# Optimization experiments

Measured on AMD Instinct MI355X. Metric: run time of the kernel, lower is better.

Reference implementation:

```python
import jax, jax.numpy as jnp
import numpy as np

B, N, F, H, K, C = 2048, 62, 512, 128, 2, 2
EPS_BN = 1e-5
EPS_NORM = 1e-10
N_TRIL = N * (N + 1) // 2  # 1953, tril_indices incl. diagonal
FC_SIZES = [H * N, H * N // 2, H * N // 4, H * N // 8, C]  # [7936,3968,1984,992,2]


def setup_inputs() -> dict:
    key = jax.random.key(0)
    ks = jax.random.split(key, 16)
    inp = {
        "x": jax.random.normal(ks[0], (B, N, F), jnp.float32),
        "edge_weight": jax.random.uniform(ks[1], (N_TRIL,), jnp.float32),
        "bn_gamma": jnp.ones((F,), jnp.float32),
        "bn_beta": jnp.zeros((F,), jnp.float32),
        # xavier_normal for SGConv lin
        "lin_w": jax.random.normal(ks[2], (H, F), jnp.float32) * (2.0 / (F + H)) ** 0.5,
        "lin_b": jnp.zeros((H,), jnp.float32),
    }
    for i in range(4):
        fan_in, fan_out = FC_SIZES[i], FC_SIZES[i + 1]
        inp[f"fc{i}_w"] = jax.random.normal(ks[3 + i], (fan_out, fan_in), jnp.float32) * (2.0 / (fan_in + fan_out)) ** 0.5
        inp[f"fc{i}_b"] = jnp.zeros((fan_out,), jnp.float32)
    return inp


def _normalized_adj(edge_weight):
    """Build symmetric dense adjacency from tril params, normalize_matrix
    (relu + sym deg-norm), then SGConv.norm (D^-1/2 A D^-1/2; self-loops are
    already on the diagonal so add_remaining_self_loops is a no-op)."""
    xs, ys = np.tril_indices(N)
    Wm = jnp.zeros((N, N), jnp.float32).at[xs, ys].set(edge_weight)
    Wm = Wm + Wm.T - jnp.diag(jnp.diag(Wm))
    A = jax.nn.relu(Wm)
    dinv = jax.lax.rsqrt(A.sum(1) + EPS_NORM)
    A = dinv[:, None] * A * dinv[None, :]
    # SGConv normalization: deg = scatter_add over rows -> row sums
    deg = A.sum(1)
    dis = jnp.where(deg > 0, deg ** -0.5, 0.0)
    return dis[:, None] * A * dis[None, :]


def reference(x, edge_weight, bn_gamma, bn_beta, lin_w, lin_b,
              fc0_w, fc0_b, fc1_w, fc1_b, fc2_w, fc2_b, fc3_w, fc3_b):
    A = _normalized_adj(edge_weight)  # [N, N], shared across batch
    # BatchNorm1d over feature channels, stats over (batch, node) dims (train mode)
    mean = x.mean((0, 1))
    var = x.var((0, 1))
    h = (x - mean) * jax.lax.rsqrt(var + EPS_BN) * bn_gamma + bn_beta  # [B,N,F]
    # K-hop SGConv propagation == dense matmul with shared normalized adjacency
    for _ in range(K):
        h = jnp.einsum('ij,bjf->bif', A, h)
    h = h @ lin_w.T + lin_b           # [B, N, H]
    h = h.reshape(B, N * H)           # node-major flatten, matches x.view(batch,-1)
    # dropout is identity in eval mode
    for W, b in ((fc0_w, fc0_b), (fc1_w, fc1_b), (fc2_w, fc2_b)):
        h = jax.nn.relu(h @ W.T + b)
    return h @ fc3_w.T + fc3_b        # [B, C]
```

## Files before the change

kernel.cpp:

```cpp
#include <hip/hip_runtime.h>

typedef _Float16 f16;
typedef __attribute__((ext_vector_type(4))) _Float16 f16x4;
typedef __attribute__((ext_vector_type(8))) _Float16 f16x8;
typedef __attribute__((ext_vector_type(4))) float f32x4;

#define DEVI static __device__ __forceinline__

DEVI void async_copy16(const f16* g, f16* l) {
  __builtin_amdgcn_global_load_lds(
      (const __attribute__((address_space(1))) void*)g,
      (__attribute__((address_space(3))) void*)l, 16, 0, 0);
}

#define MEMPIN asm volatile("" ::: "memory")
#define RBAR __builtin_amdgcn_s_barrier()

__global__ __launch_bounds__(1024) void k_adj(const float* __restrict__ ew, float* __restrict__ out)
{
  __shared__ float sW[62][64];
  __shared__ float sT[62][64];
  __shared__ float d[62];
  const int tid = threadIdx.x;
  for (int idx = tid; idx < 62 * 62; idx += 1024) {
    int i = idx / 62, j = idx % 62;
    float w = (j <= i) ? ew[i * (i + 1) / 2 + j] : ew[j * (j + 1) / 2 + i];
    sW[i][j] = fmaxf(w, 0.f);
  }
  __syncthreads();
  if (tid < 62) {
    float s = 0.f;
    for (int j = 0; j < 62; j++) s += sW[tid][j];
    d[tid] = rsqrtf(s + 1e-10f);
  }
  __syncthreads();
  for (int idx = tid; idx < 62 * 62; idx += 1024) {
    int i = idx / 62, j = idx % 62;
    sW[i][j] *= d[i] * d[j];
  }
  __syncthreads();
  if (tid < 62) {
    float s = 0.f;
    for (int j = 0; j < 62; j++) s += sW[tid][j];
    d[tid] = (s > 0.f) ? rsqrtf(s) : 0.f;
  }
  __syncthreads();
  for (int idx = tid; idx < 62 * 62; idx += 1024) {
    int i = idx / 62, j = idx % 62;
    sW[i][j] *= d[i] * d[j];
  }
  __syncthreads();
  for (int idx = tid; idx < 62 * 64; idx += 1024) {
    int i = idx >> 6, j = idx & 63;
    float s = 0.f;
    if (j < 62) {
      for (int k = 0; k < 62; k++) s += sW[i][k] * sW[k][j];
    }
    sT[i][j] = s;
    out[idx] = s;
  }
  __syncthreads();
  if (tid < 62) {
    float s = 0.f;
    for (int j = 0; j < 62; j++) s += sT[tid][j];
    out[62 * 64 + tid] = s;
  }
}

__global__ __launch_bounds__(1024) void k_bnstats(const float* __restrict__ X, float* __restrict__ part)
{
  const int tid = threadIdx.x;
  const int c4 = (tid & 127) << 2;
  const int rg = tid >> 7;
  float sx = 0, sy = 0, sz = 0, sw = 0, qx = 0, qy = 0, qz = 0, qw = 0;
  const long r0 = (long)blockIdx.x * 496 + rg;
  for (int i = 0; i < 62; i++) {
    const float4 v = *(const float4*)(X + (r0 + 8 * i) * 512 + c4);
    sx += v.x; sy += v.y; sz += v.z; sw += v.w;
    qx += v.x * v.x; qy += v.y * v.y; qz += v.z * v.z; qw += v.w * v.w;
  }
  __shared__ float red[1024][8];
  red[tid][0] = sx; red[tid][1] = sy; red[tid][2] = sz; red[tid][3] = sw;
  red[tid][4] = qx; red[tid][5] = qy; red[tid][6] = qz; red[tid][7] = qw;
  __syncthreads();
  if (tid < 128) {
    float acc8[8];
#pragma unroll
    for (int j = 0; j < 8; j++) acc8[j] = 0.f;
#pragma unroll
    for (int g = 0; g < 8; g++)
#pragma unroll
      for (int j = 0; j < 8; j++) acc8[j] += red[g * 128 + tid][j];
    float* p = part + (long)blockIdx.x * 1024;
#pragma unroll
    for (int j = 0; j < 4; j++) p[c4 + j] = acc8[j];
#pragma unroll
    for (int j = 0; j < 4; j++) p[512 + c4 + j] = acc8[4 + j];
  }
}

__global__ __launch_bounds__(512) void k_bnfin(const float* __restrict__ part, const float* __restrict__ g,
                                               const float* __restrict__ be, float* __restrict__ ssb)
{
  const int c = threadIdx.x;
  float s = 0.f, q = 0.f;
  for (int b = 0; b < 256; b++) {
    s += part[b * 1024 + c];
    q += part[b * 1024 + 512 + c];
  }
  const float inv = 1.f / 126976.f;
  const float mean = s * inv;
  const float var = q * inv - mean * mean;
  const float sc = g[c] * rsqrtf(var + 1e-5f);
  ssb[c] = sc;
  ssb[512 + c] = be[c] - mean * sc;
}

__global__ __launch_bounds__(256) void k_foldw1(const float* __restrict__ lw, const float* __restrict__ ssb,
                                                f16* __restrict__ w1h, float* __restrict__ b1p)
{
  const int h = blockIdx.x;
  const int tid = threadIdx.x;
  float partl = 0.f;
  for (int f = tid; f < 512; f += 256) {
    const float w = lw[h * 512 + f];
    w1h[h * 512 + f] = (f16)(w * ssb[f]);
    partl += w * ssb[512 + f];
  }
  __shared__ float red[256];
  red[tid] = partl;
  __syncthreads();
  for (int s = 128; s; s >>= 1) {
    if (tid < s) red[tid] += red[tid + s];
    __syncthreads();
  }
  if (tid == 0) b1p[h] = red[0];
}

__global__ __launch_bounds__(256) void k_cvtw(const float* __restrict__ src, f16* __restrict__ dst,
                                              int N, int K, int Npad, int Kpad)
{
  const long total4 = (long)Npad * Kpad / 4;
  const int kp4 = Kpad >> 2;
  for (long i = (long)blockIdx.x * 256 + threadIdx.x; i < total4; i += (long)gridDim.x * 256) {
    const long n = i / kp4;
    const int k = (int)(i % kp4) << 2;
    f16x4 h;
    if (n < N && k < K) {
      const float4 v = *(const float4*)(src + n * K + k);
      h[0] = (f16)v.x; h[1] = (f16)v.y; h[2] = (f16)v.z; h[3] = (f16)v.w;
    } else {
      h[0] = (f16)0.f; h[1] = (f16)0.f; h[2] = (f16)0.f; h[3] = (f16)0.f;
    }
    *(f16x4*)(dst + i * 4) = h;
  }
}

__global__ __launch_bounds__(256, 4) void k_gemm_lin(
    const float* __restrict__ X, const f16* __restrict__ Bw, f16* __restrict__ Y)
{
  __shared__ f16 sA[128 * 64];
  __shared__ f16 sB[128 * 64];
  const int tid = threadIdx.x;
  const int lane = tid & 63;
  const int wave = tid >> 6;
  const int wr = wave >> 1, wc = wave & 1;
  const long rowA0 = (long)blockIdx.x * 128;

  const int srow = tid >> 3;
  const int scolb = (tid & 7) << 4;
  const int gcolb = scolb ^ ((srow & 7) << 4);
  const f16* gB = Bw + (long)srow * 512 + (gcolb >> 1);
  f16* lB = sB + srow * 64 + (scolb >> 1);

  const int ac4 = tid & 15;
  const int ar0 = tid >> 4;
  const int aswz = (ar0 & 7) << 4;
  const float* gX = X + (rowA0 + ar0) * 512 + ac4 * 4;
  char* lAbase = (char*)sA + ar0 * 128 + ((ac4 * 8) ^ aswz);

  const int frow = lane & 15;
  const int kb = (lane >> 4) << 4;
  const int rswz = (lane & 7) << 4;

  f32x4 acc[4][4] = {};

  for (int kt = 0; kt < 512; kt += 64) {
#pragma unroll
    for (int i = 0; i < 8; i++) {
      const float4 v = *(const float4*)(gX + kt + (long)(16 * i) * 512);
      f16x4 hh;
      hh[0] = (f16)v.x; hh[1] = (f16)v.y; hh[2] = (f16)v.z; hh[3] = (f16)v.w;
      *(f16x4*)(lAbase + 16 * i * 128) = hh;
    }
#pragma unroll
    for (int i = 0; i < 4; i++)
      async_copy16(gB + kt + (long)i * (32 * 512), lB + i * 2048);
    __syncthreads();
#pragma unroll
    for (int kk = 0; kk < 2; kk++) {
      f16x8 af[4], bf[4];
#pragma unroll
      for (int m = 0; m < 4; m++) {
        const int row = wr * 64 + m * 16 + frow;
        af[m] = *(const f16x8*)((const char*)sA + row * 128 + ((kk * 64 + kb) ^ rswz));
      }
#pragma unroll
      for (int n = 0; n < 4; n++) {
        const int row = wc * 64 + n * 16 + frow;
        bf[n] = *(const f16x8*)((const char*)sB + row * 128 + ((kk * 64 + kb) ^ rswz));
      }
#pragma unroll
      for (int m = 0; m < 4; m++)
#pragma unroll
        for (int n = 0; n < 4; n++)
          acc[m][n] = __builtin_amdgcn_mfma_f32_16x16x32_f16(af[m], bf[n], acc[m][n], 0, 0, 0);
    }
    __syncthreads();
  }

  const int crow = wr * 64 + ((lane >> 4) << 2);
  const int ccol = wc * 64 + (lane & 15);
#pragma unroll
  for (int n = 0; n < 4; n++) {
    const int col = ccol + n * 16;
#pragma unroll
    for (int m = 0; m < 4; m++) {
      const long gr = rowA0 + crow + m * 16;
#pragma unroll
      for (int r = 0; r < 4; r++)
        Y[(gr + r) * 128 + col] = (f16)acc[m][n][r];
    }
  }
}

__global__ __launch_bounds__(256) void k_prop(const f16* __restrict__ Y, const float* __restrict__ A2,
                                              const float* __restrict__ b1p, const float* __restrict__ lb,
                                              f16* __restrict__ Z)
{
  __shared__ float sY[62 * 128];
  __shared__ float sA[62 * 64];
  __shared__ float sR[62];
  __shared__ float sB1[128];
  __shared__ float sLB[128];
  const int tid = threadIdx.x;
  const long base = (long)blockIdx.x * 7936;
  for (int i = tid; i < 992; i += 256) {
    const f16x8 v = *(const f16x8*)(Y + base + (long)i * 8);
#pragma unroll
    for (int j = 0; j < 8; j++) sY[i * 8 + j] = (float)v[j];
    const float4 a = *(const float4*)(A2 + i * 4);
    *(float4*)&sA[i * 4] = a;
  }
  if (tid < 62) sR[tid] = A2[3968 + tid];
  if (tid >= 64 && tid < 192) sB1[tid - 64] = b1p[tid - 64];
  if (tid >= 128 && tid < 256) sLB[tid - 128] = lb[tid - 128];
  __syncthreads();
  const int h = tid & 127;
  const int ng = tid >> 7;
  float yc[62];
#pragma unroll
  for (int j = 0; j < 62; j++) yc[j] = sY[j * 128 + h];
  const float bias_h1 = sB1[h];
  const float bias_h2 = sLB[h];
  for (int n = ng; n < 62; n += 2) {
    float s = 0.f;
#pragma unroll
    for (int j = 0; j < 62; j++) s += sA[n * 64 + j] * yc[j];
    s += sR[n] * bias_h1 + bias_h2;
    Z[base + n * 128 + h] = (f16)s;
  }
}

template <int LOOPN, int MT, int NT, int KS>
__global__ __launch_bounds__(512, 2) void k_fc8(
    const f16* __restrict__ A, const f16* __restrict__ Bw, f16* __restrict__ P,
    const int K, const int kslice, const int PLD)
{
  __shared__ f16 sA[2][256 * 64];
  __shared__ f16 sB[2][256 * 64];
  const int tid = threadIdx.x;
  const int bid = blockIdx.x;
  const int xcd = bid & 7, ii = bid >> 3;
  int nt, mt, ks;
  if constexpr (NT == 16) {
    nt = xcd * 2 + (ii & 1); mt = (ii >> 1) & (MT - 1); ks = ii >> 4;
  } else {
    nt = xcd; mt = ii & (MT - 1); ks = ii >> 3;
  }
  const long rowA0 = (long)mt * 256;
  const long rowB0 = (long)nt * 256;
  const long k0 = (long)ks * kslice;

  const int srow = tid >> 3;
  const int scolb = (tid & 7) << 4;
  const int gcolb = scolb ^ ((srow & 7) << 4);
  const f16* gA = A + (rowA0 + srow) * (long)K + k0 + (gcolb >> 1);
  const f16* gB = Bw + (rowB0 + srow) * (long)K + k0 + (gcolb >> 1);

#define SGA(d, q, kt) async_copy16(gA + (kt) + (long)(q) * 64 * K, &sA[d][0] + (q) * 4096 + tid * 8)
#define SGB(d, q, kt) async_copy16(gB + (kt) + (long)(q) * 64 * K, &sB[d][0] + (q) * 4096 + tid * 8)

  const int lane = tid & 63;
  const int wave = tid >> 6;
  const int wr = wave >> 2;
  const int wc = wave & 3;
  const int frow = lane & 15;
  const int kb = (lane >> 4) << 4;
  const int rsw = (frow & 7) << 4;

  f32x4 acc[8][4] = {};
  f16x8 af[4][2], bf[4][2];

#define RDA(d, mh) do { _Pragma("unroll") for (int m_ = 0; m_ < 4; m_++) {                      \
    const int row_ = wr * 128 + (mh) * 64 + m_ * 16 + frow;                                     \
    af[m_][0] = *(const f16x8*)((const char*)&sA[d][0] + row_ * 128 + ((0 + kb) ^ rsw));        \
    af[m_][1] = *(const f16x8*)((const char*)&sA[d][0] + row_ * 128 + ((64 + kb) ^ rsw)); } } while (0)
#define RDB(d) do { _Pragma("unroll") for (int n_ = 0; n_ < 4; n_++) {                          \
    const int row_ = wc * 64 + n_ * 16 + frow;                                                  \
    bf[n_][0] = *(const f16x8*)((const char*)&sB[d][0] + row_ * 128 + ((0 + kb) ^ rsw));        \
    bf[n_][1] = *(const f16x8*)((const char*)&sB[d][0] + row_ * 128 + ((64 + kb) ^ rsw)); } } while (0)
#define QUAD(mh, nh) do { _Pragma("unroll") for (int m_ = 0; m_ < 4; m_++)                      \
    _Pragma("unroll") for (int n_ = 0; n_ < 2; n_++) {                                          \
      acc[(mh)*4+m_][(nh)*2+n_] = __builtin_amdgcn_mfma_f32_16x16x32_f16(af[m_][0], bf[(nh)*2+n_][0], acc[(mh)*4+m_][(nh)*2+n_], 0, 0, 0); \
      acc[(mh)*4+m_][(nh)*2+n_] = __builtin_amdgcn_mfma_f32_16x16x32_f16(af[m_][1], bf[(nh)*2+n_][1], acc[(mh)*4+m_][(nh)*2+n_], 0, 0, 0); } } while (0)
#define VMW8 asm volatile("s_waitcnt vmcnt(8)" ::: "memory")
#define VMW0 asm volatile("s_waitcnt vmcnt(0)" ::: "memory")
#define PRIO1 __builtin_amdgcn_s_setprio(1)
#define PRIO0 __builtin_amdgcn_s_setprio(0)

  SGA(0, 0, 0); SGA(0, 2, 0); SGB(0, 0, 0); SGB(0, 1, 0);
  SGA(0, 1, 0); SGA(0, 3, 0); SGB(0, 2, 0); SGB(0, 3, 0);
  SGA(1, 0, 64); SGA(1, 2, 64); SGB(1, 0, 64); SGB(1, 1, 64);
  SGA(1, 1, 64); SGA(1, 3, 64); SGB(1, 2, 64); SGB(1, 3, 64);

  for (int t = 0; t < LOOPN; ++t) {
    const long kt2 = (long)(t + 1) * 128;
    VMW8; MEMPIN; RBAR; MEMPIN;
    RDA(0, 0); RDB(0);
    PRIO1; QUAD(0, 0); PRIO0;
    MEMPIN; RBAR; MEMPIN;
    SGA(0, 0, kt2); SGA(0, 2, kt2); SGB(0, 0, kt2); SGB(0, 1, kt2);
    QUAD(0, 1);
    RDA(0, 1);
    QUAD(1, 0);
    MEMPIN; RBAR; MEMPIN;
    SGA(0, 1, kt2); SGA(0, 3, kt2); SGB(0, 2, kt2); SGB(0, 3, kt2);
    QUAD(1, 1);
    VMW8; MEMPIN; RBAR; MEMPIN;
    RDA(1, 0); RDB(1);
    PRIO1; QUAD(0, 0); PRIO0;
    MEMPIN; RBAR; MEMPIN;
    SGA(1, 0, kt2 + 64); SGA(1, 2, kt2 + 64); SGB(1, 0, kt2 + 64); SGB(1, 1, kt2 + 64);
    QUAD(0, 1);
    RDA(1, 1);
    QUAD(1, 0);
    MEMPIN; RBAR; MEMPIN;
    SGA(1, 1, kt2 + 64); SGA(1, 3, kt2 + 64); SGB(1, 2, kt2 + 64); SGB(1, 3, kt2 + 64);
    QUAD(1, 1);
  }
  VMW8; MEMPIN; RBAR; MEMPIN;
  RDA(0, 0); RDB(0);
  PRIO1; QUAD(0, 0); QUAD(0, 1); PRIO0;
  RDA(0, 1);
  PRIO1; QUAD(1, 0); QUAD(1, 1); PRIO0;
  VMW0; MEMPIN; RBAR; MEMPIN;
  RDA(1, 0); RDB(1);
  PRIO1; QUAD(0, 0); QUAD(0, 1); PRIO0;
  RDA(1, 1);
  PRIO1; QUAD(1, 0); QUAD(1, 1); PRIO0;

  f16* Pp = P + (long)ks * 2048 * PLD;
#pragma unroll
  for (int mi = 0; mi < 8; mi++) {
    const long r0 = rowA0 + wr * 128 + (mi >> 2) * 64 + (mi & 3) * 16 + ((lane >> 4) << 2);
#pragma unroll
    for (int n = 0; n < 4; n++) {
      const long col = rowB0 + wc * 64 + n * 16 + (lane & 15);
#pragma unroll
      for (int r = 0; r < 4; r++)
        Pp[(r0 + r) * PLD + col] = (f16)acc[mi][n][r];
    }
  }
#undef SGA
#undef SGB
#undef RDA
#undef RDB
#undef QUAD
#undef VMW8
#undef VMW0
#undef PRIO1
#undef PRIO0
}

template <int S>
__global__ __launch_bounds__(256) void k_fixs(const f16* __restrict__ P, const float* __restrict__ b,
                                              f16* __restrict__ C, int N, int realN)
{
  const long total = 2048L * N;
  const int mask = N - 1;
  const long stride = (long)gridDim.x * 256 * 8;
  for (long i = ((long)blockIdx.x * 256 + threadIdx.x) * 8; i < total; i += stride) {
    float s[8];
#pragma unroll
    for (int j = 0; j < 8; j++) s[j] = 0.f;
#pragma unroll
    for (int ps = 0; ps < S; ps++) {
      const f16x8 p = *(const f16x8*)(P + (long)ps * total + i);
#pragma unroll
      for (int j = 0; j < 8; j++) s[j] += (float)p[j];
    }
    const int col = (int)(i & mask);
    f16x8 o;
#pragma unroll
    for (int j = 0; j < 8; j++) {
      const int c = col + j;
      const float bb = (c < realN) ? b[c] : 0.f;
      o[j] = (f16)fmaxf(s[j] + bb, 0.f);
    }
    *(f16x8*)(C + i) = o;
  }
}

template <int RELU>
__global__ __launch_bounds__(256, 2) void k_gemm_f16(
    const f16* __restrict__ A, const f16* __restrict__ B,
    const float* __restrict__ bias, f16* __restrict__ C,
    int N, int K, int realN)
{
  __shared__ f16 sA[128 * 64];
  __shared__ f16 sB[128 * 64];
  const int tid = threadIdx.x;
  const int lane = tid & 63;
  const int wave = tid >> 6;
  const int wr = wave >> 1, wc = wave & 1;
  const int bid = blockIdx.x;
  const int xcd = bid & 7, idx = bid >> 3;
  const long rowA0 = (long)(xcd * 2 + (idx & 1)) * 128;
  const long rowB0 = (long)(idx >> 1) * 128;

  const int srow = tid >> 3;
  const int scolb = (tid & 7) << 4;
  const int gcolb = scolb ^ ((srow & 7) << 4);
  const f16* gA = A + (rowA0 + srow) * (long)K + (gcolb >> 1);
  const f16* gB = B + (rowB0 + srow) * (long)K + (gcolb >> 1);
  f16* lA = sA + srow * 64 + (scolb >> 1);
  f16* lB = sB + srow * 64 + (scolb >> 1);
  const long rstep = 32L * K;

  const int frow = lane & 15;
  const int kb = (lane >> 4) << 4;
  const int rswz = (lane & 7) << 4;

  f32x4 acc[4][4] = {};

  for (int kt = 0; kt < K; kt += 64) {
#pragma unroll
    for (int i = 0; i < 4; i++) {
      async_copy16(gA + kt + i * rstep, lA + i * 2048);
      async_copy16(gB + kt + i * rstep, lB + i * 2048);
    }
    __syncthreads();
#pragma unroll
    for (int kk = 0; kk < 2; kk++) {
      f16x8 af[4], bf[4];
#pragma unroll
      for (int m = 0; m < 4; m++) {
        const int row = wr * 64 + m * 16 + frow;
        af[m] = *(const f16x8*)((const char*)sA + row * 128 + ((kk * 64 + kb) ^ rswz));
      }
#pragma unroll
      for (int n = 0; n < 4; n++) {
        const int row = wc * 64 + n * 16 + frow;
        bf[n] = *(const f16x8*)((const char*)sB + row * 128 + ((kk * 64 + kb) ^ rswz));
      }
#pragma unroll
      for (int m = 0; m < 4; m++)
#pragma unroll
        for (int n = 0; n < 4; n++)
          acc[m][n] = __builtin_amdgcn_mfma_f32_16x16x32_f16(af[m], bf[n], acc[m][n], 0, 0, 0);
    }
    __syncthreads();
  }

  const int crow = wr * 64 + ((lane >> 4) << 2);
  const int ccol = wc * 64 + (lane & 15);
#pragma unroll
  for (int n = 0; n < 4; n++) {
    const int col = (int)rowB0 + ccol + n * 16;
    const float bb = (col < realN) ? bias[col] : 0.f;
#pragma unroll
    for (int m = 0; m < 4; m++) {
      const long gr = rowA0 + crow + m * 16;
#pragma unroll
      for (int r = 0; r < 4; r++) {
        float v = acc[m][n][r] + bb;
        if (RELU) v = fmaxf(v, 0.f);
        C[(gr + r) * N + col] = (f16)v;
      }
    }
  }
}

__global__ __launch_bounds__(256) void k_fc3(const f16* __restrict__ H, const float* __restrict__ W,
                                             const float* __restrict__ b, float* __restrict__ out)
{
  const int row = blockIdx.x * 4 + (threadIdx.x >> 6);
  const int lane = threadIdx.x & 63;
  const f16* h = H + (long)row * 1024;
  float a0 = 0.f, a1 = 0.f;
  for (int k = lane; k < 992; k += 64) {
    const float v = (float)h[k];
    a0 += v * W[k];
    a1 += v * W[992 + k];
  }
  for (int off = 32; off; off >>= 1) {
    a0 += __shfl_down(a0, off);
    a1 += __shfl_down(a1, off);
  }
  if (lane == 0) {
    out[row * 2 + 0] = a0 + b[0];
    out[row * 2 + 1] = a1 + b[1];
  }
}

extern "C" void kernel_launch(void* const* d_in, const int* in_sizes, int n_in,
                              void* d_out, int out_size, void* d_ws, size_t ws_size,
                              hipStream_t stream)
{
  const float* x    = (const float*)d_in[0];
  const float* ew   = (const float*)d_in[1];
  const float* bng  = (const float*)d_in[2];
  const float* bnb  = (const float*)d_in[3];
  const float* linw = (const float*)d_in[4];
  const float* linb = (const float*)d_in[5];
  const float* w0   = (const float*)d_in[6];
  const float* b0   = (const float*)d_in[7];
  const float* w1   = (const float*)d_in[8];
  const float* b1   = (const float*)d_in[9];
  const float* w2   = (const float*)d_in[10];
  const float* b2   = (const float*)d_in[11];
  const float* w3   = (const float*)d_in[12];
  const float* b3   = (const float*)d_in[13];
  float* out = (float*)d_out;
  char* ws = (char*)d_ws;

  constexpr size_t oA2  = 0;
  constexpr size_t oSS  = 16384;
  constexpr size_t oB1P = 20480;
  constexpr size_t oW1H = 20992;
  constexpr size_t oP   = 152064;
  constexpr size_t oACC = oP;
  constexpr size_t oY   = oP + 1048576;
  constexpr size_t oZ   = 33706496;
  constexpr size_t oW0H = 66212352;
  constexpr size_t WS_NEED = 131224064;
  constexpr size_t oH0  = oZ;
  constexpr size_t oW1F = oZ + 16777216;
  constexpr size_t oH1  = 67260928;
  constexpr size_t oW2F = 75649536;
  constexpr size_t oH2  = 79843840;
  if (ws_size < WS_NEED) return;

  float* A2  = (float*)(ws + oA2);
  float* acc = (float*)(ws + oACC);
  float* ssb = (float*)(ws + oSS);
  float* b1p = (float*)(ws + oB1P);
  f16* w1h = (f16*)(ws + oW1H);
  f16* Y   = (f16*)(ws + oY);
  f16* P   = (f16*)(ws + oP);
  f16* Z   = (f16*)(ws + oZ);
  f16* w0h = (f16*)(ws + oW0H);
  f16* h0  = (f16*)(ws + oH0);
  f16* w1f = (f16*)(ws + oW1F);
  f16* h1  = (f16*)(ws + oH1);
  f16* w2f = (f16*)(ws + oW2F);
  f16* h2  = (f16*)(ws + oH2);

  k_adj<<<1, 1024, 0, stream>>>(ew, A2);
  k_bnstats<<<256, 1024, 0, stream>>>(x, acc);
  k_bnfin<<<1, 512, 0, stream>>>(acc, bng, bnb, ssb);
  k_foldw1<<<128, 256, 0, stream>>>(linw, ssb, w1h, b1p);
  k_cvtw<<<1024, 256, 0, stream>>>(w0, w0h, 3968, 7936, 4096, 7936);
  k_gemm_lin<<<992, 256, 0, stream>>>(x, w1h, Y);
  k_prop<<<2048, 256, 0, stream>>>(Y, A2, b1p, linb, Z);
  k_fc8<30, 8, 16, 2><<<256, 512, 0, stream>>>(Z, w0h, P, 7936, 3968, 4096);
  k_fixs<2><<<2048, 256, 0, stream>>>(P, b0, h0, 4096, 3968);
  k_cvtw<<<512, 256, 0, stream>>>(w1, w1f, 1984, 3968, 2048, 4096);
  k_cvtw<<<256, 256, 0, stream>>>(w2, w2f, 992, 1984, 1024, 2048);
  k_fc8<7, 8, 8, 4><<<256, 512, 0, stream>>>(h0, w1f, P, 4096, 1024, 2048);
  k_fixs<4><<<1024, 256, 0, stream>>>(P, b1, h1, 2048, 1984);
  k_gemm_f16<1><<<128, 256, 0, stream>>>(h1, w2f, b2, h2, 1024, 2048, 992);
  k_fc3<<<512, 256, 0, stream>>>(h2, w3, b3, out);
}
```

Measured before the change: 504.7 us.

## Restructure FC GEMM main loop into eight-phase ping-pong schedule with finer B reads

Rewrites the double-buffered MFMA main loop of the FC split-K GEMM into eight phases per iteration. Each phase reads half of the B fragments, issues a pair of async global-to-LDS loads, and runs one MFMA quadrant between barriers. The B fragment register array shrinks from four tiles to two, and the wait threshold drops to vmcnt(4). The aim is to interleave loads, LDS reads and MFMAs more finely and lower register pressure, at the cost of many more workgroup barriers and extra B fragment reloads.

```diff
diff --git a/kernel.cpp b/kernel.cpp
--- a/kernel.cpp
+++ b/kernel.cpp
@@ -300,6 +300,10 @@
 
 #define SGA(d, q, kt) async_copy16(gA + (kt) + (long)(q) * 64 * K, &sA[d][0] + (q) * 4096 + tid * 8)
 #define SGB(d, q, kt) async_copy16(gB + (kt) + (long)(q) * 64 * K, &sB[d][0] + (q) * 4096 + tid * 8)
+#define SA02(d, kt) do { SGA(d, 0, kt); SGA(d, 2, kt); } while (0)
+#define SA13(d, kt) do { SGA(d, 1, kt); SGA(d, 3, kt); } while (0)
+#define SB01(d, kt) do { SGB(d, 0, kt); SGB(d, 1, kt); } while (0)
+#define SB23(d, kt) do { SGB(d, 2, kt); SGB(d, 3, kt); } while (0)
 
   const int lane = tid & 63;
   const int wave = tid >> 6;
@@ -310,65 +314,71 @@
   const int rsw = (frow & 7) << 4;
 
   f32x4 acc[8][4] = {};
-  f16x8 af[4][2], bf[4][2];
-
-#define RDA(d, mh) do { _Pragma("unroll") for (int m_ = 0; m_ < 4; m_++) {                      \
+  f16x8 af[4][2], bf[2][2];
+
+#define RDA8(d, mh) do { _Pragma("unroll") for (int m_ = 0; m_ < 4; m_++) {                     \
     const int row_ = wr * 128 + (mh) * 64 + m_ * 16 + frow;                                     \
-    af[m_][0] = *(const f16x8*)((const char*)&sA[d][0] + row_ * 128 + ((0 + kb) ^ rsw));        \
+    af[m_][0] = *(const f16x8*)((const char*)&sA[d][0] + row_ * 128 + (kb ^ rsw));              \
     af[m_][1] = *(const f16x8*)((const char*)&sA[d][0] + row_ * 128 + ((64 + kb) ^ rsw)); } } while (0)
-#define RDB(d) do { _Pragma("unroll") for (int n_ = 0; n_ < 4; n_++) {                          \
-    const int row_ = wc * 64 + n_ * 16 + frow;                                                  \
-    bf[n_][0] = *(const f16x8*)((const char*)&sB[d][0] + row_ * 128 + ((0 + kb) ^ rsw));        \
+#define RDB4(d, nh) do { _Pragma("unroll") for (int n_ = 0; n_ < 2; n_++) {                     \
+    const int row_ = wc * 64 + (nh) * 32 + n_ * 16 + frow;                                      \
+    bf[n_][0] = *(const f16x8*)((const char*)&sB[d][0] + row_ * 128 + (kb ^ rsw));              \
     bf[n_][1] = *(const f16x8*)((const char*)&sB[d][0] + row_ * 128 + ((64 + kb) ^ rsw)); } } while (0)
-#define QUAD(mh, nh) do { _Pragma("unroll") for (int m_ = 0; m_ < 4; m_++)                      \
+#define QUAD8(mh, nh) do { _Pragma("unroll") for (int m_ = 0; m_ < 4; m_++)                     \
     _Pragma("unroll") for (int n_ = 0; n_ < 2; n_++) {                                          \
-      acc[(mh)*4+m_][(nh)*2+n_] = __builtin_amdgcn_mfma_f32_16x16x32_f16(af[m_][0], bf[(nh)*2+n_][0], acc[(mh)*4+m_][(nh)*2+n_], 0, 0, 0); \
-      acc[(mh)*4+m_][(nh)*2+n_] = __builtin_amdgcn_mfma_f32_16x16x32_f16(af[m_][1], bf[(nh)*2+n_][1], acc[(mh)*4+m_][(nh)*2+n_], 0, 0, 0); } } while (0)
-#define VMW8 asm volatile("s_waitcnt vmcnt(8)" ::: "memory")
+      acc[(mh)*4+m_][(nh)*2+n_] = __builtin_amdgcn_mfma_f32_16x16x32_f16(af[m_][0], bf[n_][0], acc[(mh)*4+m_][(nh)*2+n_], 0, 0, 0); \
+      acc[(mh)*4+m_][(nh)*2+n_] = __builtin_amdgcn_mfma_f32_16x16x32_f16(af[m_][1], bf[n_][1], acc[(mh)*4+m_][(nh)*2+n_], 0, 0, 0); } } while (0)
+#define VMW4 asm volatile("s_waitcnt vmcnt(4)" ::: "memory")
 #define VMW0 asm volatile("s_waitcnt vmcnt(0)" ::: "memory")
 #define PRIO1 __builtin_amdgcn_s_setprio(1)
 #define PRIO0 __builtin_amdgcn_s_setprio(0)
-
-  SGA(0, 0, 0); SGA(0, 2, 0); SGB(0, 0, 0); SGB(0, 1, 0);
-  SGA(0, 1, 0); SGA(0, 3, 0); SGB(0, 2, 0); SGB(0, 3, 0);
-  SGA(1, 0, 64); SGA(1, 2, 64); SGB(1, 0, 64); SGB(1, 1, 64);
-  SGA(1, 1, 64); SGA(1, 3, 64); SGB(1, 2, 64); SGB(1, 3, 64);
+#define BAR1 do { MEMPIN; RBAR; MEMPIN; } while (0)
+
+  SA02(0, 0); SA13(0, 0); SB01(0, 0); SB23(0, 0);
+  SA02(1, 64); SA13(1, 64);
+  VMW4; BAR1;
 
   for (int t = 0; t < LOOPN; ++t) {
-    const long kt2 = (long)(t + 1) * 128;
-    VMW8; MEMPIN; RBAR; MEMPIN;
-    RDA(0, 0); RDB(0);
-    PRIO1; QUAD(0, 0); PRIO0;
-    MEMPIN; RBAR; MEMPIN;
-    SGA(0, 0, kt2); SGA(0, 2, kt2); SGB(0, 0, kt2); SGB(0, 1, kt2);
-    QUAD(0, 1);
-    RDA(0, 1);
-    QUAD(1, 0);
-    MEMPIN; RBAR; MEMPIN;
-    SGA(0, 1, kt2); SGA(0, 3, kt2); SGB(0, 2, kt2); SGB(0, 3, kt2);
-    QUAD(1, 1);
-    VMW8; MEMPIN; RBAR; MEMPIN;
-    RDA(1, 0); RDB(1);
-    PRIO1; QUAD(0, 0); PRIO0;
-    MEMPIN; RBAR; MEMPIN;
-    SGA(1, 0, kt2 + 64); SGA(1, 2, kt2 + 64); SGB(1, 0, kt2 + 64); SGB(1, 1, kt2 + 64);
-    QUAD(0, 1);
-    RDA(1, 1);
-    QUAD(1, 0);
-    MEMPIN; RBAR; MEMPIN;
-    SGA(1, 1, kt2 + 64); SGA(1, 3, kt2 + 64); SGB(1, 2, kt2 + 64); SGB(1, 3, kt2 + 64);
-    QUAD(1, 1);
-  }
-  VMW8; MEMPIN; RBAR; MEMPIN;
-  RDA(0, 0); RDB(0);
-  PRIO1; QUAD(0, 0); QUAD(0, 1); PRIO0;
-  RDA(0, 1);
-  PRIO1; QUAD(1, 0); QUAD(1, 1); PRIO0;
-  VMW0; MEMPIN; RBAR; MEMPIN;
-  RDA(1, 0); RDB(1);
-  PRIO1; QUAD(0, 0); QUAD(0, 1); PRIO0;
-  RDA(1, 1);
-  PRIO1; QUAD(1, 0); QUAD(1, 1); PRIO0;
+    const long ktB1 = (long)t * 128 + 64;
+    const long ktN  = (long)(t + 1) * 128;
+    const long ktN1 = ktN + 64;
+    RDA8(0, 0); RDB4(0, 0); SB01(1, ktB1);
+    BAR1; PRIO1; QUAD8(0, 0); PRIO0; BAR1;
+    RDB4(0, 1); SB23(1, ktB1);
+    BAR1; PRIO1; QUAD8(0, 1); PRIO0; BAR1;
+    RDA8(0, 1); RDB4(0, 0); SA02(0, ktN);
+    BAR1; PRIO1; QUAD8(1, 0); PRIO0; BAR1;
+    RDB4(0, 1); SA13(0, ktN);
+    BAR1; PRIO1; QUAD8(1, 1); PRIO0; VMW4; BAR1;
+    RDA8(1, 0); RDB4(1, 0); SB01(0, ktN);
+    BAR1; PRIO1; QUAD8(0, 0); PRIO0; BAR1;
+    RDB4(1, 1); SB23(0, ktN);
+    BAR1; PRIO1; QUAD8(0, 1); PRIO0; BAR1;
+    RDA8(1, 1); RDB4(1, 0); SA02(1, ktN1);
+    BAR1; PRIO1; QUAD8(1, 0); PRIO0; BAR1;
+    RDB4(1, 1); SA13(1, ktN1);
+    BAR1; PRIO1; QUAD8(1, 1); PRIO0; VMW4; BAR1;
+  }
+
+  {
+    const long ktB1 = (long)LOOPN * 128 + 64;
+    RDA8(0, 0); RDB4(0, 0); SB01(1, ktB1);
+    BAR1; PRIO1; QUAD8(0, 0); PRIO0; BAR1;
+    RDB4(0, 1); SB23(1, ktB1);
+    BAR1; PRIO1; QUAD8(0, 1); PRIO0; BAR1;
+    RDA8(0, 1); RDB4(0, 0);
+    BAR1; PRIO1; QUAD8(1, 0); PRIO0; BAR1;
+    RDB4(0, 1);
+    BAR1; PRIO1; QUAD8(1, 1); PRIO0; VMW0; BAR1;
+    RDA8(1, 0); RDB4(1, 0);
+    PRIO1; QUAD8(0, 0); PRIO0;
+    RDB4(1, 1);
+    PRIO1; QUAD8(0, 1); PRIO0;
+    RDA8(1, 1); RDB4(1, 0);
+    PRIO1; QUAD8(1, 0); PRIO0;
+    RDB4(1, 1);
+    PRIO1; QUAD8(1, 1); PRIO0;
+  }
 
   f16* Pp = P + (long)ks * 2048 * PLD;
 #pragma unroll
@@ -384,13 +394,18 @@
   }
 #undef SGA
 #undef SGB
-#undef RDA
-#undef RDB
-#undef QUAD
-#undef VMW8
+#undef SA02
+#undef SA13
+#undef SB01
+#undef SB23
+#undef RDA8
+#undef RDB4
+#undef QUAD8
+#undef VMW4
 #undef VMW0
 #undef PRIO1
 #undef PRIO0
+#undef BAR1
 }
 
 template <int S>
```

Result: slower. 534.1 us (+5.8%).

## Fuse linear projection GEMM with adjacency propagation into one kernel

Applied to the files above, without the earlier changes.

Merges k_gemm_lin and k_prop into k_linprop. Each block computes 124 rows (two full batch samples) of the X·W1 projection with MFMA, stages the f16 result in shared memory, then applies the shared 62x62 adjacency and biases directly before writing Z. This removes the Y intermediate round trip through global memory and one kernel launch. In exchange, 4 of each 128 tile rows are wasted (clamped loads), and shared memory use rises, lowering occupancy to 2 blocks per CU.

```diff
diff --git a/kernel.cpp b/kernel.cpp
--- a/kernel.cpp
+++ b/kernel.cpp
@@ -156,16 +156,29 @@
   }
 }
 
-__global__ __launch_bounds__(256, 4) void k_gemm_lin(
-    const float* __restrict__ X, const f16* __restrict__ Bw, f16* __restrict__ Y)
-{
-  __shared__ f16 sA[128 * 64];
-  __shared__ f16 sB[128 * 64];
+__global__ __launch_bounds__(256, 2) void k_linprop(
+    const float* __restrict__ X, const f16* __restrict__ Bw,
+    const float* __restrict__ A2, const float* __restrict__ b1p,
+    const float* __restrict__ lb, f16* __restrict__ Z)
+{
+  __shared__ f16 smem[128 * 128];
+  __shared__ float sA2[62 * 64];
+  __shared__ float sR[62];
+  __shared__ float sB1[128];
+  __shared__ float sLB[128];
+  f16* sA = smem;
+  f16* sB = smem + 8192;
   const int tid = threadIdx.x;
   const int lane = tid & 63;
   const int wave = tid >> 6;
   const int wr = wave >> 1, wc = wave & 1;
-  const long rowA0 = (long)blockIdx.x * 128;
+  const long rowA0 = (long)blockIdx.x * 124;
+
+  for (int i = tid; i < 992; i += 256)
+    *(float4*)&sA2[i * 4] = *(const float4*)(A2 + i * 4);
+  if (tid < 62) sR[tid] = A2[3968 + tid];
+  if (tid < 128) sB1[tid] = b1p[tid];
+  if (tid >= 128) sLB[tid - 128] = lb[tid - 128];
 
   const int srow = tid >> 3;
   const int scolb = (tid & 7) << 4;
@@ -176,7 +189,6 @@
   const int ac4 = tid & 15;
   const int ar0 = tid >> 4;
   const int aswz = (ar0 & 7) << 4;
-  const float* gX = X + (rowA0 + ar0) * 512 + ac4 * 4;
   char* lAbase = (char*)sA + ar0 * 128 + ((ac4 * 8) ^ aswz);
 
   const int frow = lane & 15;
@@ -188,7 +200,9 @@
   for (int kt = 0; kt < 512; kt += 64) {
 #pragma unroll
     for (int i = 0; i < 8; i++) {
-      const float4 v = *(const float4*)(gX + kt + (long)(16 * i) * 512);
+      long rr = rowA0 + ar0 + 16 * i;
+      if (rr > 126975) rr = 126975;
+      const float4 v = *(const float4*)(X + rr * 512 + kt + ac4 * 4);
       f16x4 hh;
       hh[0] = (f16)v.x; hh[1] = (f16)v.y; hh[2] = (f16)v.z; hh[3] = (f16)v.w;
       *(f16x4*)(lAbase + 16 * i * 128) = hh;
@@ -222,53 +236,27 @@
   const int crow = wr * 64 + ((lane >> 4) << 2);
   const int ccol = wc * 64 + (lane & 15);
 #pragma unroll
-  for (int n = 0; n < 4; n++) {
-    const int col = ccol + n * 16;
-#pragma unroll
-    for (int m = 0; m < 4; m++) {
-      const long gr = rowA0 + crow + m * 16;
+  for (int n = 0; n < 4; n++)
+#pragma unroll
+    for (int m = 0; m < 4; m++)
 #pragma unroll
       for (int r = 0; r < 4; r++)
-        Y[(gr + r) * 128 + col] = (f16)acc[m][n][r];
-    }
-  }
-}
-
-__global__ __launch_bounds__(256) void k_prop(const f16* __restrict__ Y, const float* __restrict__ A2,
-                                              const float* __restrict__ b1p, const float* __restrict__ lb,
-                                              f16* __restrict__ Z)
-{
-  __shared__ float sY[62 * 128];
-  __shared__ float sA[62 * 64];
-  __shared__ float sR[62];
-  __shared__ float sB1[128];
-  __shared__ float sLB[128];
-  const int tid = threadIdx.x;
-  const long base = (long)blockIdx.x * 7936;
-  for (int i = tid; i < 992; i += 256) {
-    const f16x8 v = *(const f16x8*)(Y + base + (long)i * 8);
-#pragma unroll
-    for (int j = 0; j < 8; j++) sY[i * 8 + j] = (float)v[j];
-    const float4 a = *(const float4*)(A2 + i * 4);
-    *(float4*)&sA[i * 4] = a;
-  }
-  if (tid < 62) sR[tid] = A2[3968 + tid];
-  if (tid >= 64 && tid < 192) sB1[tid - 64] = b1p[tid - 64];
-  if (tid >= 128 && tid < 256) sLB[tid - 128] = lb[tid - 128];
-  __syncthreads();
+        smem[(crow + m * 16 + r) * 128 + ccol + n * 16] = (f16)acc[m][n][r];
+  __syncthreads();
+
   const int h = tid & 127;
-  const int ng = tid >> 7;
+  const int g = tid >> 7;
   float yc[62];
 #pragma unroll
-  for (int j = 0; j < 62; j++) yc[j] = sY[j * 128 + h];
-  const float bias_h1 = sB1[h];
-  const float bias_h2 = sLB[h];
-  for (int n = ng; n < 62; n += 2) {
+  for (int j = 0; j < 62; j++) yc[j] = (float)smem[(g * 62 + j) * 128 + h];
+  const float bh1 = sB1[h];
+  const float bh2 = sLB[h];
+  f16* zp = Z + ((long)blockIdx.x * 2 + g) * 7936 + h;
+  for (int n = 0; n < 62; n++) {
     float s = 0.f;
 #pragma unroll
-    for (int j = 0; j < 62; j++) s += sA[n * 64 + j] * yc[j];
-    s += sR[n] * bias_h1 + bias_h2;
-    Z[base + n * 128 + h] = (f16)s;
+    for (int j = 0; j < 62; j++) s += sA2[n * 64 + j] * yc[j];
+    zp[n * 128] = (f16)(s + sR[n] * bh1 + bh2);
   }
 }
 
@@ -314,11 +302,11 @@
 
 #define RDA(d, mh) do { _Pragma("unroll") for (int m_ = 0; m_ < 4; m_++) {                      \
     const int row_ = wr * 128 + (mh) * 64 + m_ * 16 + frow;                                     \
-    af[m_][0] = *(const f16x8*)((const char*)&sA[d][0] + row_ * 128 + ((0 + kb) ^ rsw));        \
+    af[m_][0] = *(const f16x8*)((const char*)&sA[d][0] + row_ * 128 + (kb ^ rsw));              \
     af[m_][1] = *(const f16x8*)((const char*)&sA[d][0] + row_ * 128 + ((64 + kb) ^ rsw)); } } while (0)
 #define RDB(d) do { _Pragma("unroll") for (int n_ = 0; n_ < 4; n_++) {                          \
     const int row_ = wc * 64 + n_ * 16 + frow;                                                  \
-    bf[n_][0] = *(const f16x8*)((const char*)&sB[d][0] + row_ * 128 + ((0 + kb) ^ rsw));        \
+    bf[n_][0] = *(const f16x8*)((const char*)&sB[d][0] + row_ * 128 + (kb ^ rsw));              \
     bf[n_][1] = *(const f16x8*)((const char*)&sB[d][0] + row_ * 128 + ((64 + kb) ^ rsw)); } } while (0)
 #define QUAD(mh, nh) do { _Pragma("unroll") for (int m_ = 0; m_ < 4; m_++)                      \
     _Pragma("unroll") for (int n_ = 0; n_ < 2; n_++) {                                          \
@@ -551,7 +539,6 @@
   constexpr size_t oW1H = 20992;
   constexpr size_t oP   = 152064;
   constexpr size_t oACC = oP;
-  constexpr size_t oY   = oP + 1048576;
   constexpr size_t oZ   = 33706496;
   constexpr size_t oW0H = 66212352;
   constexpr size_t WS_NEED = 131224064;
@@ -567,7 +554,6 @@
   float* ssb = (float*)(ws + oSS);
   float* b1p = (float*)(ws + oB1P);
   f16* w1h = (f16*)(ws + oW1H);
-  f16* Y   = (f16*)(ws + oY);
   f16* P   = (f16*)(ws + oP);
   f16* Z   = (f16*)(ws + oZ);
   f16* w0h = (f16*)(ws + oW0H);
@@ -582,8 +568,7 @@
   k_bnfin<<<1, 512, 0, stream>>>(acc, bng, bnb, ssb);
   k_foldw1<<<128, 256, 0, stream>>>(linw, ssb, w1h, b1p);
   k_cvtw<<<1024, 256, 0, stream>>>(w0, w0h, 3968, 7936, 4096, 7936);
-  k_gemm_lin<<<992, 256, 0, stream>>>(x, w1h, Y);
-  k_prop<<<2048, 256, 0, stream>>>(Y, A2, b1p, linb, Z);
+  k_linprop<<<1024, 256, 0, stream>>>(x, w1h, A2, b1p, linb, Z);
   k_fc8<30, 8, 16, 2><<<256, 512, 0, stream>>>(Z, w0h, P, 7936, 3968, 4096);
   k_fixs<2><<<2048, 256, 0, stream>>>(P, b0, h0, 4096, 3968);
   k_cvtw<<<512, 256, 0, stream>>>(w1, w1f, 1984, 3968, 2048, 4096);
```

Measured after the change: 475.2 us. -5.8%, faster.
